# Kernel optimization log

Hardware: AMD Instinct MI355X
Metric: run time of the kernel (lower is better)

The kernel has to match this reference:

```python
import jax, jax.numpy as jnp
import numpy as np

N_NODES = 50000
N_EDGES = 800000
FEAT = 128
HID = 64
N_CLS = 12


def setup_inputs() -> dict:
    key = jax.random.key(0)
    ks = jax.random.split(key, 8)
    x = jax.random.normal(ks[0], (N_NODES, FEAT), dtype=jnp.float32)
    edge_index = jax.random.randint(ks[1], (2, N_EDGES), 0, N_NODES, dtype=jnp.int64)
    s1 = 1.0 / np.sqrt(FEAT)
    s2 = 1.0 / np.sqrt(HID)
    W1 = jax.random.uniform(ks[2], (FEAT, HID), jnp.float32, -s1, s1)
    b1 = jnp.zeros((HID,), jnp.float32)
    W2 = jax.random.uniform(ks[3], (HID, HID), jnp.float32, -s2, s2)
    b2 = jnp.zeros((HID,), jnp.float32)
    Wfc = jax.random.uniform(ks[4], (HID, N_CLS), jnp.float32, -s2, s2)
    bfc = jax.random.uniform(ks[5], (N_CLS,), jnp.float32, -s2, s2)
    return {"x": x, "edge_index": edge_index, "W1": W1, "b1": b1,
            "W2": W2, "b2": b2, "Wfc": Wfc, "bfc": bfc}


def gcn_conv(x, W, b, src, dst, n_nodes):
    """PyG GCNConv: symmetric-normalized aggregation with self-loops.
    out_i = sum_{j in N(i)} (xW)_j / sqrt(d_i d_j) + (xW)_i / d_i + b,
    where d = in-degree + 1 (self loop)."""
    xw = x @ W  # [N, out] -- transform before propagate (PyG order)
    deg = jnp.zeros((n_nodes,), x.dtype).at[dst].add(1.0) + 1.0
    dinv = jax.lax.rsqrt(deg)
    norm = dinv[src] * dinv[dst]  # [E]
    agg = jax.ops.segment_sum(xw[src] * norm[:, None], dst, num_segments=n_nodes)
    agg = agg + xw * (dinv * dinv)[:, None]  # self-loop term
    return agg + b


def reference(x, edge_index, W1, b1, W2, b2, Wfc, bfc):
    n = x.shape[0]
    src, dst = edge_index[0], edge_index[1]
    h = jax.nn.relu(gcn_conv(x, W1, b1, src, dst, n))
    h = jax.nn.relu(gcn_conv(h, W2, b2, src, dst, n))
    return h @ Wfc + bfc  # [N, num_content_categories]
```

## Files before the change

### kernel.cpp

```cpp
#include <hip/hip_runtime.h>
#include <hip/hip_fp16.h>


#define CAP   64
#define NBUK  196
#define ET    4096
#define NB    196

typedef unsigned short u16;

__global__ __launch_bounds__(256) void k_hist(const int* __restrict__ dst,
                                              int* __restrict__ blkcnt, int E) {
    __shared__ int hist[NBUK];
    const int tid = threadIdx.x, blk = blockIdx.x;
    for (int i = tid; i < NBUK; i += 256) hist[i] = 0;
    __syncthreads();
    const int e0 = blk * ET;
    if (e0 + ET <= E) {
        const int4* d4 = (const int4*)(dst + e0);
#pragma unroll
        for (int j = 0; j < ET / 1024; j++) {
            int4 d = d4[j * 256 + tid];
            atomicAdd(&hist[(unsigned)d.x >> 8], 1);
            atomicAdd(&hist[(unsigned)d.y >> 8], 1);
            atomicAdd(&hist[(unsigned)d.z >> 8], 1);
            atomicAdd(&hist[(unsigned)d.w >> 8], 1);
        }
    } else {
        for (int j = 0; j < ET / 256; j++) {
            int e = e0 + j * 256 + tid;
            if (e < E) atomicAdd(&hist[(unsigned)dst[e] >> 8], 1);
        }
    }
    __syncthreads();
    for (int b = tid; b < NBUK; b += 256) blkcnt[b * NB + blk] = hist[b];
}

__global__ __launch_bounds__(256) void k_scanA(int* __restrict__ blkcnt,
                                               int* __restrict__ btot) {
    __shared__ int s[256];
    const int t = threadIdx.x, b = blockIdx.x;
    int v = (t < NB) ? blkcnt[b * NB + t] : 0;
    s[t] = v;
    __syncthreads();
#pragma unroll
    for (int d = 1; d < 256; d <<= 1) {
        int u = (t >= d) ? s[t - d] : 0;
        __syncthreads();
        s[t] += u;
        __syncthreads();
    }
    if (t < NB) blkcnt[b * NB + t] = s[t] - v;
    if (t == 255) btot[b] = s[255];
}

__device__ __forceinline__ void local_bucket_scan(const int* __restrict__ btot,
                                                  int* bb, int tid) {
    if (tid < 256) bb[tid] = (tid < NBUK) ? btot[tid] : 0;
    __syncthreads();
#pragma unroll
    for (int d = 1; d < 256; d <<= 1) {
        int u = 0;
        if (tid < 256 && tid >= d) u = bb[tid - d];
        __syncthreads();
        if (tid < 256) bb[tid] += u;
        __syncthreads();
    }
    if (tid < 256) bb[tid] -= (tid < NBUK) ? btot[tid] : 0;
    __syncthreads();
}

__global__ __launch_bounds__(256) void k_scatter(const int* __restrict__ src,
                                                 const int* __restrict__ dst,
                                                 const int* __restrict__ blkcnt,
                                                 const int* __restrict__ btot,
                                                 unsigned* __restrict__ eb, int E) {
    __shared__ int bb[256];
    __shared__ int cur[NBUK];
    const int tid = threadIdx.x, blk = blockIdx.x;
    local_bucket_scan(btot, bb, tid);
    for (int i = tid; i < NBUK; i += 256) cur[i] = blkcnt[i * NB + blk] + bb[i];
    __syncthreads();
    const int e0 = blk * ET;
    if (e0 + ET <= E) {
        const int4* s4 = (const int4*)(src + e0);
        const int4* d4 = (const int4*)(dst + e0);
#pragma unroll
        for (int j = 0; j < ET / 1024; j++) {
            int4 sv = s4[j * 256 + tid];
            int4 dv = d4[j * 256 + tid];
            unsigned u0 = ((unsigned)dv.x << 16) | (unsigned)sv.x;
            unsigned u1 = ((unsigned)dv.y << 16) | (unsigned)sv.y;
            unsigned u2 = ((unsigned)dv.z << 16) | (unsigned)sv.z;
            unsigned u3 = ((unsigned)dv.w << 16) | (unsigned)sv.w;
            eb[atomicAdd(&cur[u0 >> 24], 1)] = u0;
            eb[atomicAdd(&cur[u1 >> 24], 1)] = u1;
            eb[atomicAdd(&cur[u2 >> 24], 1)] = u2;
            eb[atomicAdd(&cur[u3 >> 24], 1)] = u3;
        }
    } else {
        for (int j = 0; j < ET / 256; j++) {
            int e = e0 + j * 256 + tid;
            if (e < E) {
                unsigned d = (unsigned)dst[e];
                unsigned u = (d << 16) | (unsigned)src[e];
                eb[atomicAdd(&cur[d >> 8], 1)] = u;
            }
        }
    }
}

__global__ __launch_bounds__(1024) void k_buildb(const unsigned* __restrict__ eb,
                                                 const int* __restrict__ btot,
                                                 u16* __restrict__ csr,
                                                 int* __restrict__ cnt, int n) {
    __shared__ int bb[256];
    __shared__ u16 lcsr[256 * CAP];
    __shared__ int cur[256];
    const int tid = threadIdx.x, b = blockIdx.x;
    local_bucket_scan(btot, bb, tid);
    if (tid < 256) cur[tid] = 0;
    __syncthreads();
    const int e0 = bb[b], e1 = bb[b] + btot[b];
    for (int e = e0 + tid; e < e1; e += 1024) {
        unsigned u = eb[e];
        int ld = (int)((u >> 16) & 255u);
        int p = atomicAdd(&cur[ld], 1);
        if (p < CAP) lcsr[ld * CAP + p] = (u16)(u & 0xffffu);
    }
    __syncthreads();
    const int node0 = b * 256;
    for (int i = tid; i < 256 * CAP / 8; i += 1024) {
        int r = i / (CAP / 8), q = i % (CAP / 8);
        int c = cur[r] < CAP ? cur[r] : CAP;
        uint4 v = *(uint4*)&lcsr[r * CAP + q * 8];
        if (q * 8 >= c) v = make_uint4(0, 0, 0, 0);
        *(uint4*)&csr[(size_t)(node0 + r) * CAP + q * 8] = v;
    }
    if (tid < 256 && node0 + tid < n) cnt[node0 + tid] = cur[tid];
}

template <int K, bool IS_HALF, typename TIN>
__global__ __launch_bounds__(256) void k_gemm(const TIN* __restrict__ X,
                                              const float* __restrict__ W,
                                              const int* __restrict__ cnt,
                                              __half* __restrict__ Y, int n) {
    constexpr int KC = 64;
    constexpr int XS = KC + 4;
    __shared__ float ws[KC * 64];
    __shared__ float xs[64 * XS];
    const int tid = threadIdx.x;
    const int tx = tid & 15;
    const int ty = tid >> 4;
    const int row0 = blockIdx.x * 64;

    float acc[4][4];
#pragma unroll
    for (int r = 0; r < 4; r++)
#pragma unroll
        for (int c = 0; c < 4; c++) acc[r][c] = 0.f;

#pragma unroll 1
    for (int kc = 0; kc < K; kc += KC) {
        for (int i = tid; i < KC * 16; i += 256) {
            int kk = i >> 4, c4 = i & 15;
            *(float4*)&ws[kk * 64 + 4 * c4] = *(const float4*)&W[(kc + kk) * 64 + 4 * c4];
        }
        if (IS_HALF) {
            for (int i = tid; i < 64 * (KC / 8); i += 256) {
                int r = i >> 3, q = i & 7;
                uint4 u = make_uint4(0, 0, 0, 0);
                int row = row0 + r;
                if (row < n) u = *(const uint4*)&X[(size_t)row * K + kc + 8 * q];
                float2 f0 = __half22float2(*(__half2*)&u.x);
                float2 f1 = __half22float2(*(__half2*)&u.y);
                float2 f2 = __half22float2(*(__half2*)&u.z);
                float2 f3 = __half22float2(*(__half2*)&u.w);
                *(float4*)&xs[r * XS + 8 * q]     = make_float4(f0.x, f0.y, f1.x, f1.y);
                *(float4*)&xs[r * XS + 8 * q + 4] = make_float4(f2.x, f2.y, f3.x, f3.y);
            }
        } else {
            for (int i = tid; i < 64 * (KC / 4); i += 256) {
                int r = i / (KC / 4), q = i % (KC / 4);
                float4 v = make_float4(0.f, 0.f, 0.f, 0.f);
                int row = row0 + r;
                if (row < n) v = *(const float4*)&((const float*)X)[(size_t)row * K + kc + 4 * q];
                *(float4*)&xs[r * XS + 4 * q] = v;
            }
        }
        __syncthreads();

#pragma unroll 2
        for (int q = 0; q < KC / 4; q++) {
            float4 xv[4];
#pragma unroll
            for (int r = 0; r < 4; r++)
                xv[r] = *(const float4*)&xs[(ty + 16 * r) * XS + 4 * q];
#pragma unroll
            for (int kk = 0; kk < 4; kk++) {
                float4 wv = *(const float4*)&ws[(4 * q + kk) * 64 + 4 * tx];
#pragma unroll
                for (int r = 0; r < 4; r++) {
                    float xval = (kk == 0) ? xv[r].x : (kk == 1) ? xv[r].y
                               : (kk == 2) ? xv[r].z : xv[r].w;
                    acc[r][0] = fmaf(xval, wv.x, acc[r][0]);
                    acc[r][1] = fmaf(xval, wv.y, acc[r][1]);
                    acc[r][2] = fmaf(xval, wv.z, acc[r][2]);
                    acc[r][3] = fmaf(xval, wv.w, acc[r][3]);
                }
            }
        }
        __syncthreads();
    }

#pragma unroll
    for (int r = 0; r < 4; r++) {
        int row = row0 + ty + 16 * r;
        if (row < n) {
            float d = rsqrtf((float)cnt[row] + 1.0f);
            __half2* yh = (__half2*)&Y[(size_t)row * 64 + 4 * tx];
            yh[0] = __floats2half2_rn(acc[r][0] * d, acc[r][1] * d);
            yh[1] = __floats2half2_rn(acc[r][2] * d, acc[r][3] * d);
        }
    }
}

__device__ __forceinline__ float4 gather_node(const __half* __restrict__ y,
                                              const u16* __restrict__ lst,
                                              int deg, int c4) {
    float4 a0 = make_float4(0.f, 0.f, 0.f, 0.f);
    float4 a1 = make_float4(0.f, 0.f, 0.f, 0.f);
    int i = 0;
    for (; i + 16 <= deg; i += 16) {
        uint4 qa = *(const uint4*)(lst + i);
        uint4 qb = *(const uint4*)(lst + i + 8);
        unsigned idx[16] = {qa.x & 0xffffu, qa.x >> 16, qa.y & 0xffffu, qa.y >> 16,
                            qa.z & 0xffffu, qa.z >> 16, qa.w & 0xffffu, qa.w >> 16,
                            qb.x & 0xffffu, qb.x >> 16, qb.y & 0xffffu, qb.y >> 16,
                            qb.z & 0xffffu, qb.z >> 16, qb.w & 0xffffu, qb.w >> 16};
        uint2 v[16];
#pragma unroll
        for (int t = 0; t < 16; t++) v[t] = *(const uint2*)&y[idx[t] * 64 + 4 * c4];
#pragma unroll
        for (int t = 0; t < 16; t += 2) {
            float2 lo0 = __half22float2(*(__half2*)&v[t].x);
            float2 hi0 = __half22float2(*(__half2*)&v[t].y);
            float2 lo1 = __half22float2(*(__half2*)&v[t + 1].x);
            float2 hi1 = __half22float2(*(__half2*)&v[t + 1].y);
            a0.x += lo0.x; a0.y += lo0.y; a0.z += hi0.x; a0.w += hi0.y;
            a1.x += lo1.x; a1.y += lo1.y; a1.z += hi1.x; a1.w += hi1.y;
        }
    }
    if (i + 8 <= deg) {
        uint4 qa = *(const uint4*)(lst + i);
        unsigned idx[8] = {qa.x & 0xffffu, qa.x >> 16, qa.y & 0xffffu, qa.y >> 16,
                           qa.z & 0xffffu, qa.z >> 16, qa.w & 0xffffu, qa.w >> 16};
        uint2 v[8];
#pragma unroll
        for (int t = 0; t < 8; t++) v[t] = *(const uint2*)&y[idx[t] * 64 + 4 * c4];
#pragma unroll
        for (int t = 0; t < 8; t += 2) {
            float2 lo0 = __half22float2(*(__half2*)&v[t].x);
            float2 hi0 = __half22float2(*(__half2*)&v[t].y);
            float2 lo1 = __half22float2(*(__half2*)&v[t + 1].x);
            float2 hi1 = __half22float2(*(__half2*)&v[t + 1].y);
            a0.x += lo0.x; a0.y += lo0.y; a0.z += hi0.x; a0.w += hi0.y;
            a1.x += lo1.x; a1.y += lo1.y; a1.z += hi1.x; a1.w += hi1.y;
        }
        i += 8;
    }
    if (i + 4 <= deg) {
        uint2 qa = *(const uint2*)(lst + i);
        unsigned idx[4] = {qa.x & 0xffffu, qa.x >> 16, qa.y & 0xffffu, qa.y >> 16};
        uint2 v[4];
#pragma unroll
        for (int t = 0; t < 4; t++) v[t] = *(const uint2*)&y[idx[t] * 64 + 4 * c4];
#pragma unroll
        for (int t = 0; t < 4; t += 2) {
            float2 lo0 = __half22float2(*(__half2*)&v[t].x);
            float2 hi0 = __half22float2(*(__half2*)&v[t].y);
            float2 lo1 = __half22float2(*(__half2*)&v[t + 1].x);
            float2 hi1 = __half22float2(*(__half2*)&v[t + 1].y);
            a0.x += lo0.x; a0.y += lo0.y; a0.z += hi0.x; a0.w += hi0.y;
            a1.x += lo1.x; a1.y += lo1.y; a1.z += hi1.x; a1.w += hi1.y;
        }
        i += 4;
    }
    for (; i < deg; i++) {
        uint2 vv = *(const uint2*)&y[lst[i] * 64 + 4 * c4];
        float2 lo = __half22float2(*(__half2*)&vv.x);
        float2 hi = __half22float2(*(__half2*)&vv.y);
        a0.x += lo.x; a0.y += lo.y; a0.z += hi.x; a0.w += hi.y;
    }
    return make_float4(a0.x + a1.x, a0.y + a1.y, a0.z + a1.z, a0.w + a1.w);
}

__global__ __launch_bounds__(256) void k_agg1(const __half* __restrict__ y,
                                              const u16* __restrict__ csr,
                                              const int* __restrict__ cnt,
                                              const float* __restrict__ bias,
                                              __half* __restrict__ h1, int n) {
    const int tid = threadIdx.x;
    const int c4 = tid & 15;
    const int node = blockIdx.x * 16 + (tid >> 4);
    if (node >= n) return;
    int deg_raw = cnt[node];
    int deg = deg_raw > CAP ? CAP : deg_raw;
    float4 acc = gather_node(y, csr + node * CAP, deg, c4);
    uint2 sv = *(const uint2*)&y[node * 64 + 4 * c4];
    float2 slo = __half22float2(*(__half2*)&sv.x);
    float2 shi = __half22float2(*(__half2*)&sv.y);
    float d = rsqrtf((float)deg_raw + 1.0f);
    float4 bv = *(const float4*)&bias[4 * c4];
    float v0 = fmaxf(fmaf(d, acc.x + slo.x, bv.x), 0.f);
    float v1 = fmaxf(fmaf(d, acc.y + slo.y, bv.y), 0.f);
    float v2 = fmaxf(fmaf(d, acc.z + shi.x, bv.z), 0.f);
    float v3 = fmaxf(fmaf(d, acc.w + shi.y, bv.w), 0.f);
    uint2 o;
    *(__half2*)&o.x = __floats2half2_rn(v0, v1);
    *(__half2*)&o.y = __floats2half2_rn(v2, v3);
    *(uint2*)&h1[node * 64 + 4 * c4] = o;
}

__global__ __launch_bounds__(256) void k_agg2fc(const __half* __restrict__ y,
                                                const u16* __restrict__ csr,
                                                const int* __restrict__ cnt,
                                                const float* __restrict__ bias,
                                                const float* __restrict__ Wfc,
                                                const float* __restrict__ bfc,
                                                float* __restrict__ out, int n) {
    __shared__ float wf[12 * 64];
    __shared__ float bf[12];
    const int tid = threadIdx.x;
    for (int i = tid; i < 12 * 64; i += 256) {
        int c = i >> 6, k = i & 63;
        wf[i] = Wfc[k * 12 + c];
    }
    if (tid < 12) bf[tid] = bfc[tid];
    __syncthreads();

    const int c4 = tid & 15;
    const int node = blockIdx.x * 16 + (tid >> 4);
    if (node >= n) return;
    int deg_raw = cnt[node];
    int deg = deg_raw > CAP ? CAP : deg_raw;
    float4 acc = gather_node(y, csr + node * CAP, deg, c4);
    uint2 sv = *(const uint2*)&y[node * 64 + 4 * c4];
    float2 slo = __half22float2(*(__half2*)&sv.x);
    float2 shi = __half22float2(*(__half2*)&sv.y);
    float d = rsqrtf((float)deg_raw + 1.0f);
    float4 bv = *(const float4*)&bias[4 * c4];
    float v0 = fmaxf(fmaf(d, acc.x + slo.x, bv.x), 0.f);
    float v1 = fmaxf(fmaf(d, acc.y + slo.y, bv.y), 0.f);
    float v2 = fmaxf(fmaf(d, acc.z + shi.x, bv.z), 0.f);
    float v3 = fmaxf(fmaf(d, acc.w + shi.y, bv.w), 0.f);

    float res = 0.f;
#pragma unroll
    for (int c = 0; c < 12; c++) {
        float4 wv = *(const float4*)&wf[c * 64 + 4 * c4];
        float p = v0 * wv.x + v1 * wv.y + v2 * wv.z + v3 * wv.w;
        p += __shfl_xor(p, 1);
        p += __shfl_xor(p, 2);
        p += __shfl_xor(p, 4);
        p += __shfl_xor(p, 8);
        if (c4 == c) res = p + bf[c];
    }
    if (c4 < 12) out[(size_t)node * 12 + c4] = res;
}

extern "C" void kernel_launch(void* const* d_in, const int* in_sizes, int n_in,
                              void* d_out, int out_size, void* d_ws, size_t ws_size,
                              hipStream_t stream) {
    const float* x   = (const float*)d_in[0];
    const int*   ei  = (const int*)d_in[1];
    const float* W1  = (const float*)d_in[2];
    const float* b1  = (const float*)d_in[3];
    const float* W2  = (const float*)d_in[4];
    const float* b2  = (const float*)d_in[5];
    const float* Wfc = (const float*)d_in[6];
    const float* bfc = (const float*)d_in[7];
    float* out = (float*)d_out;

    const int n = in_sizes[0] / 128;
    const int E = in_sizes[1] / 2;
    const int* src = ei;
    const int* dst = ei + E;
    const int nblk = (E + ET - 1) / ET;

    char* w = (char*)d_ws;
    unsigned* eb  = (unsigned*)w;  w += (size_t)((E + 63) / 64) * 64 * 4;
    int* blkcnt   = (int*)w;       w += (size_t)NBUK * NB * 4 + 256;
    int* btot     = (int*)w;       w += 256 * 4;
    int* cnt      = (int*)w;       w += (size_t)((n + 63) / 64) * 64 * 4;
    u16* csr      = (u16*)w;       w += (size_t)NBUK * 256 * CAP * 2;
    __half* y     = (__half*)w;    w += (size_t)n * 64 * 2;
    __half* h1    = (__half*)w;

    k_hist   <<<dim3(nblk), dim3(256), 0, stream>>>(dst, blkcnt, E);
    k_scanA  <<<dim3(NBUK), dim3(256), 0, stream>>>(blkcnt, btot);
    k_scatter<<<dim3(nblk), dim3(256), 0, stream>>>(src, dst, blkcnt, btot, eb, E);
    k_buildb <<<dim3(NBUK), dim3(1024), 0, stream>>>(eb, btot, csr, cnt, n);
    k_gemm<128, false, float><<<dim3((n + 63) / 64), dim3(256), 0, stream>>>(x, W1, cnt, y, n);
    k_agg1   <<<dim3((n + 15) / 16), dim3(256), 0, stream>>>(y, csr, cnt, b1, h1, n);
    k_gemm<64, true, __half><<<dim3((n + 63) / 64), dim3(256), 0, stream>>>(h1, W2, cnt, y, n);
    k_agg2fc <<<dim3((n + 15) / 16), dim3(256), 0, stream>>>(y, csr, cnt, b2, Wfc, bfc, out, n);
}
```

Measured before the change: 186.9 us.

## Split feature columns into halves so gather aggregation fits in L2

The GEMM now writes its 64-wide fp16 output as two separate 32-column planes, and each aggregation kernel runs twice, once per plane. Each pass gathers from a table half the size, which is meant to raise L2 hit rates for the random neighbor reads. The final FC layer is split into a partial-sum pass and a combining pass that goes through a float scratch buffer. Neighbor index lists are loaded with nontemporal loads. The cost is reading the CSR lists twice, extra kernel launches, and narrower per-thread loads.

```diff
diff --git a/kernel.cpp b/kernel.cpp
--- a/kernel.cpp
+++ b/kernel.cpp
@@ -8,6 +8,7 @@
 #define NB    196
 
 typedef unsigned short u16;
+typedef unsigned long long u64;
 
 __global__ __launch_bounds__(256) void k_hist(const int* __restrict__ dst,
                                               int* __restrict__ blkcnt, int E) {
@@ -142,9 +143,11 @@
 
 template <int K, bool IS_HALF, typename TIN>
 __global__ __launch_bounds__(256) void k_gemm(const TIN* __restrict__ X,
+                                              const __half* __restrict__ X1,
                                               const float* __restrict__ W,
                                               const int* __restrict__ cnt,
-                                              __half* __restrict__ Y, int n) {
+                                              __half* __restrict__ Y,
+                                              __half* __restrict__ Y1, int n) {
     constexpr int KC = 64;
     constexpr int XS = KC + 4;
     __shared__ float ws[KC * 64];
@@ -166,12 +169,17 @@
             int kk = i >> 4, c4 = i & 15;
             *(float4*)&ws[kk * 64 + 4 * c4] = *(const float4*)&W[(kc + kk) * 64 + 4 * c4];
         }
-        if (IS_HALF) {
-            for (int i = tid; i < 64 * (KC / 8); i += 256) {
+        if constexpr (IS_HALF) {
+            const __half* Xh = (const __half*)X;
+            for (int i = tid; i < 64 * 8; i += 256) {
                 int r = i >> 3, q = i & 7;
                 uint4 u = make_uint4(0, 0, 0, 0);
                 int row = row0 + r;
-                if (row < n) u = *(const uint4*)&X[(size_t)row * K + kc + 8 * q];
+                if (row < n) {
+                    const __half* p = (q < 4) ? &Xh[(size_t)row * 32 + 8 * q]
+                                              : &X1[(size_t)row * 32 + 8 * q - 32];
+                    u = *(const uint4*)p;
+                }
                 float2 f0 = __half22float2(*(__half2*)&u.x);
                 float2 f1 = __half22float2(*(__half2*)&u.y);
                 float2 f2 = __half22float2(*(__half2*)&u.z);
@@ -180,11 +188,12 @@
                 *(float4*)&xs[r * XS + 8 * q + 4] = make_float4(f2.x, f2.y, f3.x, f3.y);
             }
         } else {
+            const float* Xf = (const float*)X;
             for (int i = tid; i < 64 * (KC / 4); i += 256) {
                 int r = i / (KC / 4), q = i % (KC / 4);
                 float4 v = make_float4(0.f, 0.f, 0.f, 0.f);
                 int row = row0 + r;
-                if (row < n) v = *(const float4*)&((const float*)X)[(size_t)row * K + kc + 4 * q];
+                if (row < n) v = *(const float4*)&Xf[(size_t)row * K + kc + 4 * q];
                 *(float4*)&xs[r * XS + 4 * q] = v;
             }
         }
@@ -218,155 +227,152 @@
         int row = row0 + ty + 16 * r;
         if (row < n) {
             float d = rsqrtf((float)cnt[row] + 1.0f);
-            __half2* yh = (__half2*)&Y[(size_t)row * 64 + 4 * tx];
-            yh[0] = __floats2half2_rn(acc[r][0] * d, acc[r][1] * d);
-            yh[1] = __floats2half2_rn(acc[r][2] * d, acc[r][3] * d);
-        }
-    }
-}
-
-__device__ __forceinline__ float4 gather_node(const __half* __restrict__ y,
-                                              const u16* __restrict__ lst,
-                                              int deg, int c4) {
-    float4 a0 = make_float4(0.f, 0.f, 0.f, 0.f);
-    float4 a1 = make_float4(0.f, 0.f, 0.f, 0.f);
+            __half2 h0 = __floats2half2_rn(acc[r][0] * d, acc[r][1] * d);
+            __half2 h1v = __floats2half2_rn(acc[r][2] * d, acc[r][3] * d);
+            uint2 o = make_uint2(*(unsigned*)&h0, *(unsigned*)&h1v);
+            if (tx < 8) *(uint2*)&Y[(size_t)row * 32 + 4 * tx] = o;
+            else        *(uint2*)&Y1[(size_t)row * 32 + 4 * tx - 32] = o;
+        }
+    }
+}
+
+__device__ __forceinline__ float2 gather32(const __half* __restrict__ yP,
+                                           const u16* __restrict__ lst,
+                                           int deg, int c2) {
+    float2 A = make_float2(0.f, 0.f), B = make_float2(0.f, 0.f);
     int i = 0;
     for (; i + 16 <= deg; i += 16) {
-        uint4 qa = *(const uint4*)(lst + i);
-        uint4 qb = *(const uint4*)(lst + i + 8);
-        unsigned idx[16] = {qa.x & 0xffffu, qa.x >> 16, qa.y & 0xffffu, qa.y >> 16,
-                            qa.z & 0xffffu, qa.z >> 16, qa.w & 0xffffu, qa.w >> 16,
-                            qb.x & 0xffffu, qb.x >> 16, qb.y & 0xffffu, qb.y >> 16,
-                            qb.z & 0xffffu, qb.z >> 16, qb.w & 0xffffu, qb.w >> 16};
-        uint2 v[16];
-#pragma unroll
-        for (int t = 0; t < 16; t++) v[t] = *(const uint2*)&y[idx[t] * 64 + 4 * c4];
+        const u64* lp = (const u64*)(lst + i);
+        u64 q0 = __builtin_nontemporal_load(lp);
+        u64 q1 = __builtin_nontemporal_load(lp + 1);
+        u64 q2 = __builtin_nontemporal_load(lp + 2);
+        u64 q3 = __builtin_nontemporal_load(lp + 3);
+        unsigned idx[16];
+#pragma unroll
+        for (int t = 0; t < 4; t++) {
+            idx[t]      = (unsigned)((q0 >> (16 * t)) & 0xffffu);
+            idx[t + 4]  = (unsigned)((q1 >> (16 * t)) & 0xffffu);
+            idx[t + 8]  = (unsigned)((q2 >> (16 * t)) & 0xffffu);
+            idx[t + 12] = (unsigned)((q3 >> (16 * t)) & 0xffffu);
+        }
+        __half2 v[16];
+#pragma unroll
+        for (int t = 0; t < 16; t++) v[t] = *(const __half2*)&yP[(size_t)idx[t] * 32 + 2 * c2];
 #pragma unroll
         for (int t = 0; t < 16; t += 2) {
-            float2 lo0 = __half22float2(*(__half2*)&v[t].x);
-            float2 hi0 = __half22float2(*(__half2*)&v[t].y);
-            float2 lo1 = __half22float2(*(__half2*)&v[t + 1].x);
-            float2 hi1 = __half22float2(*(__half2*)&v[t + 1].y);
-            a0.x += lo0.x; a0.y += lo0.y; a0.z += hi0.x; a0.w += hi0.y;
-            a1.x += lo1.x; a1.y += lo1.y; a1.z += hi1.x; a1.w += hi1.y;
+            float2 f0 = __half22float2(v[t]), f1 = __half22float2(v[t + 1]);
+            A.x += f0.x; A.y += f0.y; B.x += f1.x; B.y += f1.y;
         }
     }
     if (i + 8 <= deg) {
-        uint4 qa = *(const uint4*)(lst + i);
-        unsigned idx[8] = {qa.x & 0xffffu, qa.x >> 16, qa.y & 0xffffu, qa.y >> 16,
-                           qa.z & 0xffffu, qa.z >> 16, qa.w & 0xffffu, qa.w >> 16};
-        uint2 v[8];
-#pragma unroll
-        for (int t = 0; t < 8; t++) v[t] = *(const uint2*)&y[idx[t] * 64 + 4 * c4];
+        const u64* lp = (const u64*)(lst + i);
+        u64 q0 = __builtin_nontemporal_load(lp);
+        u64 q1 = __builtin_nontemporal_load(lp + 1);
+        unsigned idx[8];
+#pragma unroll
+        for (int t = 0; t < 4; t++) {
+            idx[t]     = (unsigned)((q0 >> (16 * t)) & 0xffffu);
+            idx[t + 4] = (unsigned)((q1 >> (16 * t)) & 0xffffu);
+        }
+        __half2 v[8];
+#pragma unroll
+        for (int t = 0; t < 8; t++) v[t] = *(const __half2*)&yP[(size_t)idx[t] * 32 + 2 * c2];
 #pragma unroll
         for (int t = 0; t < 8; t += 2) {
-            float2 lo0 = __half22float2(*(__half2*)&v[t].x);
-            float2 hi0 = __half22float2(*(__half2*)&v[t].y);
-            float2 lo1 = __half22float2(*(__half2*)&v[t + 1].x);
-            float2 hi1 = __half22float2(*(__half2*)&v[t + 1].y);
-            a0.x += lo0.x; a0.y += lo0.y; a0.z += hi0.x; a0.w += hi0.y;
-            a1.x += lo1.x; a1.y += lo1.y; a1.z += hi1.x; a1.w += hi1.y;
+            float2 f0 = __half22float2(v[t]), f1 = __half22float2(v[t + 1]);
+            A.x += f0.x; A.y += f0.y; B.x += f1.x; B.y += f1.y;
         }
         i += 8;
     }
     if (i + 4 <= deg) {
-        uint2 qa = *(const uint2*)(lst + i);
-        unsigned idx[4] = {qa.x & 0xffffu, qa.x >> 16, qa.y & 0xffffu, qa.y >> 16};
-        uint2 v[4];
-#pragma unroll
-        for (int t = 0; t < 4; t++) v[t] = *(const uint2*)&y[idx[t] * 64 + 4 * c4];
-#pragma unroll
-        for (int t = 0; t < 4; t += 2) {
-            float2 lo0 = __half22float2(*(__half2*)&v[t].x);
-            float2 hi0 = __half22float2(*(__half2*)&v[t].y);
-            float2 lo1 = __half22float2(*(__half2*)&v[t + 1].x);
-            float2 hi1 = __half22float2(*(__half2*)&v[t + 1].y);
-            a0.x += lo0.x; a0.y += lo0.y; a0.z += hi0.x; a0.w += hi0.y;
-            a1.x += lo1.x; a1.y += lo1.y; a1.z += hi1.x; a1.w += hi1.y;
-        }
+        u64 q0 = __builtin_nontemporal_load((const u64*)(lst + i));
+        unsigned idx[4];
+#pragma unroll
+        for (int t = 0; t < 4; t++) idx[t] = (unsigned)((q0 >> (16 * t)) & 0xffffu);
+        __half2 v[4];
+#pragma unroll
+        for (int t = 0; t < 4; t++) v[t] = *(const __half2*)&yP[(size_t)idx[t] * 32 + 2 * c2];
+        float2 f0 = __half22float2(v[0]), f1 = __half22float2(v[1]);
+        float2 f2 = __half22float2(v[2]), f3 = __half22float2(v[3]);
+        A.x += (f0.x + f1.x) + (f2.x + f3.x);
+        A.y += (f0.y + f1.y) + (f2.y + f3.y);
         i += 4;
     }
     for (; i < deg; i++) {
-        uint2 vv = *(const uint2*)&y[lst[i] * 64 + 4 * c4];
-        float2 lo = __half22float2(*(__half2*)&vv.x);
-        float2 hi = __half22float2(*(__half2*)&vv.y);
-        a0.x += lo.x; a0.y += lo.y; a0.z += hi.x; a0.w += hi.y;
-    }
-    return make_float4(a0.x + a1.x, a0.y + a1.y, a0.z + a1.z, a0.w + a1.w);
-}
-
-__global__ __launch_bounds__(256) void k_agg1(const __half* __restrict__ y,
+        float2 f = __half22float2(*(const __half2*)&yP[(size_t)lst[i] * 32 + 2 * c2]);
+        A.x += f.x; A.y += f.y;
+    }
+    A.x += B.x; A.y += B.y;
+    return A;
+}
+
+__global__ __launch_bounds__(256) void k_agg1(const __half* __restrict__ yP,
                                               const u16* __restrict__ csr,
                                               const int* __restrict__ cnt,
-                                              const float* __restrict__ bias,
-                                              __half* __restrict__ h1, int n) {
+                                              const float* __restrict__ biasP,
+                                              __half* __restrict__ hP, int n) {
     const int tid = threadIdx.x;
-    const int c4 = tid & 15;
+    const int c2 = tid & 15;
     const int node = blockIdx.x * 16 + (tid >> 4);
     if (node >= n) return;
     int deg_raw = cnt[node];
     int deg = deg_raw > CAP ? CAP : deg_raw;
-    float4 acc = gather_node(y, csr + node * CAP, deg, c4);
-    uint2 sv = *(const uint2*)&y[node * 64 + 4 * c4];
-    float2 slo = __half22float2(*(__half2*)&sv.x);
-    float2 shi = __half22float2(*(__half2*)&sv.y);
+    float2 acc = gather32(yP, csr + node * CAP, deg, c2);
+    float2 s = __half22float2(*(const __half2*)&yP[(size_t)node * 32 + 2 * c2]);
     float d = rsqrtf((float)deg_raw + 1.0f);
-    float4 bv = *(const float4*)&bias[4 * c4];
-    float v0 = fmaxf(fmaf(d, acc.x + slo.x, bv.x), 0.f);
-    float v1 = fmaxf(fmaf(d, acc.y + slo.y, bv.y), 0.f);
-    float v2 = fmaxf(fmaf(d, acc.z + shi.x, bv.z), 0.f);
-    float v3 = fmaxf(fmaf(d, acc.w + shi.y, bv.w), 0.f);
-    uint2 o;
-    *(__half2*)&o.x = __floats2half2_rn(v0, v1);
-    *(__half2*)&o.y = __floats2half2_rn(v2, v3);
-    *(uint2*)&h1[node * 64 + 4 * c4] = o;
-}
-
-__global__ __launch_bounds__(256) void k_agg2fc(const __half* __restrict__ y,
+    float2 bv = *(const float2*)&biasP[2 * c2];
+    float v0 = fmaxf(fmaf(d, acc.x + s.x, bv.x), 0.f);
+    float v1 = fmaxf(fmaf(d, acc.y + s.y, bv.y), 0.f);
+    __half2 o = __floats2half2_rn(v0, v1);
+    __builtin_nontemporal_store(*(unsigned*)&o, (unsigned*)&hP[(size_t)node * 32 + 2 * c2]);
+}
+
+template <int PASS>
+__global__ __launch_bounds__(256) void k_agg2fc(const __half* __restrict__ yP,
                                                 const u16* __restrict__ csr,
                                                 const int* __restrict__ cnt,
-                                                const float* __restrict__ bias,
+                                                const float* __restrict__ biasP,
                                                 const float* __restrict__ Wfc,
                                                 const float* __restrict__ bfc,
+                                                float* __restrict__ pout,
                                                 float* __restrict__ out, int n) {
-    __shared__ float wf[12 * 64];
+    __shared__ float wf[12 * 32];
     __shared__ float bf[12];
     const int tid = threadIdx.x;
-    for (int i = tid; i < 12 * 64; i += 256) {
-        int c = i >> 6, k = i & 63;
-        wf[i] = Wfc[k * 12 + c];
-    }
-    if (tid < 12) bf[tid] = bfc[tid];
-    __syncthreads();
-
-    const int c4 = tid & 15;
+    for (int i = tid; i < 12 * 32; i += 256) {
+        int c = i >> 5, k = i & 31;
+        wf[i] = Wfc[(k + 32 * PASS) * 12 + c];
+    }
+    if (PASS == 1 && tid < 12) bf[tid] = bfc[tid];
+    __syncthreads();
+
+    const int c2 = tid & 15;
     const int node = blockIdx.x * 16 + (tid >> 4);
     if (node >= n) return;
     int deg_raw = cnt[node];
     int deg = deg_raw > CAP ? CAP : deg_raw;
-    float4 acc = gather_node(y, csr + node * CAP, deg, c4);
-    uint2 sv = *(const uint2*)&y[node * 64 + 4 * c4];
-    float2 slo = __half22float2(*(__half2*)&sv.x);
-    float2 shi = __half22float2(*(__half2*)&sv.y);
+    float2 acc = gather32(yP, csr + node * CAP, deg, c2);
+    float2 s = __half22float2(*(const __half2*)&yP[(size_t)node * 32 + 2 * c2]);
     float d = rsqrtf((float)deg_raw + 1.0f);
-    float4 bv = *(const float4*)&bias[4 * c4];
-    float v0 = fmaxf(fmaf(d, acc.x + slo.x, bv.x), 0.f);
-    float v1 = fmaxf(fmaf(d, acc.y + slo.y, bv.y), 0.f);
-    float v2 = fmaxf(fmaf(d, acc.z + shi.x, bv.z), 0.f);
-    float v3 = fmaxf(fmaf(d, acc.w + shi.y, bv.w), 0.f);
+    float2 bv = *(const float2*)&biasP[2 * c2];
+    float v0 = fmaxf(fmaf(d, acc.x + s.x, bv.x), 0.f);
+    float v1 = fmaxf(fmaf(d, acc.y + s.y, bv.y), 0.f);
 
     float res = 0.f;
 #pragma unroll
     for (int c = 0; c < 12; c++) {
-        float4 wv = *(const float4*)&wf[c * 64 + 4 * c4];
-        float p = v0 * wv.x + v1 * wv.y + v2 * wv.z + v3 * wv.w;
+        float2 wv = *(const float2*)&wf[c * 32 + 2 * c2];
+        float p = v0 * wv.x + v1 * wv.y;
         p += __shfl_xor(p, 1);
         p += __shfl_xor(p, 2);
         p += __shfl_xor(p, 4);
         p += __shfl_xor(p, 8);
-        if (c4 == c) res = p + bf[c];
-    }
-    if (c4 < 12) out[(size_t)node * 12 + c4] = res;
+        if (c2 == c) res = p;
+    }
+    if (c2 < 12) {
+        if (PASS == 0) pout[(size_t)node * 12 + c2] = res;
+        else out[(size_t)node * 12 + c2] = res + pout[(size_t)node * 12 + c2] + bf[c2];
+    }
 }
 
 extern "C" void kernel_launch(void* const* d_in, const int* in_sizes, int n_in,
@@ -395,14 +401,24 @@
     int* cnt      = (int*)w;       w += (size_t)((n + 63) / 64) * 64 * 4;
     u16* csr      = (u16*)w;       w += (size_t)NBUK * 256 * CAP * 2;
     __half* y     = (__half*)w;    w += (size_t)n * 64 * 2;
-    __half* h1    = (__half*)w;
+    __half* h1    = (__half*)w;    w += (size_t)n * 64 * 2;
+    float* pout   = (float*)w;
+
+    __half* y1  = y  + (size_t)n * 32;
+    __half* h1b = h1 + (size_t)n * 32;
 
     k_hist   <<<dim3(nblk), dim3(256), 0, stream>>>(dst, blkcnt, E);
     k_scanA  <<<dim3(NBUK), dim3(256), 0, stream>>>(blkcnt, btot);
     k_scatter<<<dim3(nblk), dim3(256), 0, stream>>>(src, dst, blkcnt, btot, eb, E);
     k_buildb <<<dim3(NBUK), dim3(1024), 0, stream>>>(eb, btot, csr, cnt, n);
-    k_gemm<128, false, float><<<dim3((n + 63) / 64), dim3(256), 0, stream>>>(x, W1, cnt, y, n);
-    k_agg1   <<<dim3((n + 15) / 16), dim3(256), 0, stream>>>(y, csr, cnt, b1, h1, n);
-    k_gemm<64, true, __half><<<dim3((n + 63) / 64), dim3(256), 0, stream>>>(h1, W2, cnt, y, n);
-    k_agg2fc <<<dim3((n + 15) / 16), dim3(256), 0, stream>>>(y, csr, cnt, b2, Wfc, bfc, out, n);
-}
+    k_gemm<128, false, float><<<dim3((n + 63) / 64), dim3(256), 0, stream>>>(
+        x, (const __half*)0, W1, cnt, y, y1, n);
+    k_agg1   <<<dim3((n + 15) / 16), dim3(256), 0, stream>>>(y,  csr, cnt, b1,      h1,  n);
+    k_agg1   <<<dim3((n + 15) / 16), dim3(256), 0, stream>>>(y1, csr, cnt, b1 + 32, h1b, n);
+    k_gemm<64, true, __half><<<dim3((n + 63) / 64), dim3(256), 0, stream>>>(
+        h1, h1b, W2, cnt, y, y1, n);
+    k_agg2fc<0><<<dim3((n + 15) / 16), dim3(256), 0, stream>>>(
+        y,  csr, cnt, b2,      Wfc, bfc, pout, out, n);
+    k_agg2fc<1><<<dim3((n + 15) / 16), dim3(256), 0, stream>>>(
+        y1, csr, cnt, b2 + 32, Wfc, bfc, pout, out, n);
+}
```

New measurement: 202.3 us. 8.3% more time.
